# Kernel tuning notes

Hardware: AMD Instinct MI355X
Metric: run time of the kernel (lower is better)

The kernel has to match this reference:

```python
import jax, jax.numpy as jnp
import numpy as np
from jax import lax

# Quantization bit-widths per the module: QuantAct(16) on input,
# QuantConv2d(precision[0]=8), QuantAct(precision[0]+3=11) after relu1,
# QuantLinear(precision[1]=8).
INPUT_BIT = 16
CONV_W_BIT = 8
RELU_BIT = 11
DENSE_W_BIT = 8
EPS = 1e-8


def round_ste(x):
    # straight-through estimator rounding (HAWQ SymmetricQuantFunction)
    return x + lax.stop_gradient(jnp.round(x) - x)


def quant_act(x, bit):
    """Per-tensor symmetric dynamic activation quantization (HAWQ QuantAct).
    Returns fake-quantized x and its scaling factor."""
    n = 2 ** (bit - 1) - 1
    scale = lax.stop_gradient(jnp.maximum(jnp.max(jnp.abs(x)), EPS) / n)
    x_q = jnp.clip(round_ste(x / scale), -n, n) * scale
    return x_q, scale


def quant_weight(w, bit):
    """Per-output-channel symmetric weight quantization. w: [out, ...].
    Returns integer-valued weights and per-channel scale [out]."""
    n = 2 ** (bit - 1) - 1
    absmax = jnp.max(jnp.abs(w.reshape(w.shape[0], -1)), axis=1)
    sf = lax.stop_gradient(jnp.maximum(absmax, EPS) / n)
    bshape = (w.shape[0],) + (1,) * (w.ndim - 1)
    w_int = jnp.clip(round_ste(w / sf.reshape(bshape)), -n, n)
    return w_int, sf


def quant_conv2d(x, p_sf, w, b, bit, stride, pad):
    w_int, w_sf = quant_weight(w, bit)          # [O,I,kh,kw], [O]
    x_int = x / p_sf                            # integer-valued activations
    out_int = lax.conv_general_dilated(
        x_int, w_int, window_strides=(stride, stride),
        padding=((pad, pad), (pad, pad)),
        dimension_numbers=("NCHW", "OIHW", "NCHW"))
    bias_sf = p_sf * w_sf                       # [O]
    b_int = round_ste(b / bias_sf)
    out = (out_int + b_int[None, :, None, None]) * bias_sf[None, :, None, None]
    return out, w_sf


def quant_linear(x, p_sf, w, b, bit):
    w_int, w_sf = quant_weight(w, bit)          # [O,I], [O]
    x_int = x / p_sf
    bias_sf = p_sf * w_sf                       # [O]
    b_int = round_ste(b / bias_sf)
    out = (jnp.einsum("bi,oi->bo", x_int, w_int) + b_int[None, :]) * bias_sf[None, :]
    return out


def setup_inputs() -> dict:
    key = jax.random.key(0)
    k1, k2, k3, k4, k5 = jax.random.split(key, 5)
    B, Cin, H, W = 256, 3, 64, 64
    Cout, K = 64, 3
    Fin, Fout = Cout * 32 * 32, 256  # stride-2 conv -> 32x32 spatial
    x = jax.random.normal(k1, (B, Cin, H, W), dtype=jnp.float32)
    conv_w = jax.random.normal(k2, (Cout, Cin, K, K), dtype=jnp.float32) * 0.1
    conv_b = jax.random.normal(k3, (Cout,), dtype=jnp.float32) * 0.01
    dense_w = jax.random.normal(k4, (Fout, Fin), dtype=jnp.float32) * 0.02
    dense_b = jax.random.normal(k5, (Fout,), dtype=jnp.float32) * 0.01
    return {"x": x, "conv_w": conv_w, "conv_b": conv_b,
            "dense_w": dense_w, "dense_b": dense_b}


def reference(x, conv_w, conv_b, dense_w, dense_b):
    # x, p_sf = quant_input(x)
    xq, p_sf = quant_act(x, INPUT_BIT)
    # x, w_sf = conv(x, p_sf)
    h, w_sf = quant_conv2d(xq, p_sf, conv_w, conv_b, CONV_W_BIT, stride=2, pad=1)
    # relu1
    h = jax.nn.relu(h)
    # x, p_sf = quant_relu(x, p_sf, w_sf)  (requantize at relu_bit)
    h, p_sf = quant_act(h, RELU_BIT)
    # flatten
    h = h.reshape(h.shape[0], -1)
    # relu2(enc_dense(x, p_sf))
    out = jax.nn.relu(quant_linear(h, p_sf, dense_w, dense_b, DENSE_W_BIT))
    return out
```

## Files before the change

kernel.cpp:

```cpp
#include <hip/hip_runtime.h>
#include <hip/hip_fp16.h>
#include <cstdint>

#define B_   256
#define CIN  3
#define HW_  64
#define COUT 64
#define FIN  65536
#define FOUT 256

#define ACC_F    0
#define SC_F     65536
#define XPART_F  65552
#define WPART_F  66064
#define CSF_F    67088
#define CWINT_F  67152
#define H16_BYTE (512*1024)
#define WQ_BYTE  (H16_BYTE + 256ll*FIN*2)

typedef _Float16 half8  __attribute__((ext_vector_type(8)));
typedef _Float16 half4v __attribute__((ext_vector_type(4)));
typedef float    floatx4 __attribute__((ext_vector_type(4)));
typedef unsigned short u16;
typedef unsigned int uint_;

__device__ inline float blockMax(float v) {
    #pragma unroll
    for (int off = 32; off; off >>= 1) v = fmaxf(v, __shfl_down(v, off));
    __shared__ float sm[8];
    const int lane = threadIdx.x & 63, w = threadIdx.x >> 6;
    if (lane == 0) sm[w] = v;
    __syncthreads();
    float m = sm[0];
    const int nw = blockDim.x >> 6;
    for (int i = 1; i < nw; i++) m = fmaxf(m, sm[i]);
    return m;
}

__global__ __launch_bounds__(256) void k_stats(const float* __restrict__ x,
                                               const float* __restrict__ dw,
                                               const float* __restrict__ cw,
                                               float* __restrict__ ws) {
    const int b = blockIdx.x;
    const int t = threadIdx.x;
    if (b < 512) {
        const float4* x4 = (const float4*)x;
        float m = 0.f;
        for (int i = b * 256 + t; i < (B_ * CIN * HW_ * HW_) / 4; i += 512 * 256) {
            float4 v = x4[i];
            m = fmaxf(m, fmaxf(fmaxf(fabsf(v.x), fabsf(v.y)), fmaxf(fabsf(v.z), fabsf(v.w))));
        }
        float bm = blockMax(m);
        if (t == 0) ws[XPART_F + b] = bm;
    } else if (b < 1536) {
        const int b2 = b - 512;
        const int row = b2 >> 2, q = b2 & 3;
        const float4* r = (const float4*)(dw + (size_t)row * FIN) + q * 4096;
        float m = 0.f;
        for (int i = t; i < 4096; i += 256) {
            float4 v = r[i];
            m = fmaxf(m, fmaxf(fmaxf(fabsf(v.x), fabsf(v.y)), fmaxf(fabsf(v.z), fabsf(v.w))));
        }
        float bm = blockMax(m);
        if (t == 0) ws[WPART_F + b2] = bm;
    } else if (b == 1536) {
        if (t == 64) ((unsigned*)ws)[SC_F + 1] = 0u;
        if (t < 64) {
            const int o = t;
            float wv[27];
            float m = 0.f;
            #pragma unroll
            for (int i = 0; i < 27; i++) { wv[i] = cw[o * 27 + i]; m = fmaxf(m, fabsf(wv[i])); }
            const float sf = fmaxf(m, 1e-8f) / 127.0f;
            #pragma unroll
            for (int i = 0; i < 27; i++)
                ws[CWINT_F + o * 27 + i] = fminf(127.f, fmaxf(-127.f, rintf(wv[i] / sf)));
            ws[CSF_F + o] = sf;
        }
    } else {
        ws[ACC_F + (b - 1537) * 256 + t] = 0.f;
    }
}

__global__ __launch_bounds__(256) void k_conv(const float* __restrict__ x,
                                              const float* __restrict__ dw,
                                              const float* __restrict__ cb,
                                              const float* __restrict__ ws,
                                              u16* __restrict__ h16,
                                              signed char* __restrict__ wq,
                                              unsigned* __restrict__ maxh) {
    const int t = threadIdx.x;
    if (blockIdx.x >= 2048) {
        const int b2 = blockIdx.x - 2048;
        const int row = b2 >> 2, q = b2 & 3;
        const float* wp = ws + WPART_F + row * 4;
        const float am = fmaxf(fmaxf(wp[0], wp[1]), fmaxf(wp[2], wp[3]));
        const float inv = 127.0f / fmaxf(am, 1e-8f);
        const float4* r4 = (const float4*)(dw + (size_t)row * FIN) + q * 4096;
        uint_* wrow = (uint_*)(wq + (size_t)row * FIN) + q * 4096;
        for (int i = t; i < 4096; i += 256) {
            float4 v = r4[i];
            int q0 = (int)fminf(127.f, fmaxf(-127.f, rintf(v.x * inv)));
            int q1 = (int)fminf(127.f, fmaxf(-127.f, rintf(v.y * inv)));
            int q2 = (int)fminf(127.f, fmaxf(-127.f, rintf(v.z * inv)));
            int q3 = (int)fminf(127.f, fmaxf(-127.f, rintf(v.w * inv)));
            wrow[i] = (uint_)(q0 & 255) | ((uint_)(q1 & 255) << 8) |
                      ((uint_)(q2 & 255) << 16) | ((uint_)(q3 & 255) << 24);
        }
        return;
    }

    __shared__ float s_bsf[64], s_bint[64];
    __shared__ float xt[27 * 68];
    __shared__ float xp[256 * 28];

    float pm = fmaxf(ws[XPART_F + t], ws[XPART_F + 256 + t]);
    pm = blockMax(pm);
    const float p_sf = fmaxf(pm, 1e-8f) / 32767.0f;
    const float inv_p = 1.0f / p_sf;
    if (t < 64) {
        const float bsf = p_sf * ws[CSF_F + t];
        s_bsf[t]  = bsf;
        s_bint[t] = rintf(cb[t] / bsf);
    }

    const int b   = blockIdx.x >> 3;
    const int oyt = (blockIdx.x & 7) * 4;
    const float* xb = x + (size_t)b * (CIN * HW_ * HW_);

    for (int i = t; i < 432; i += 256) {
        const int lrow = i >> 4, c4 = i & 15;
        const int ci = lrow / 9, lr = lrow - ci * 9;
        const int iy = 2 * oyt - 1 + lr;
        float4 v = make_float4(0.f, 0.f, 0.f, 0.f);
        if ((unsigned)iy < 64u) v = *(const float4*)(xb + (ci * HW_ + iy) * HW_ + c4 * 4);
        float* d = &xt[lrow * 68 + 1 + c4 * 4];
        d[0] = fminf(32767.f, fmaxf(-32767.f, rintf(v.x * inv_p)));
        d[1] = fminf(32767.f, fmaxf(-32767.f, rintf(v.y * inv_p)));
        d[2] = fminf(32767.f, fmaxf(-32767.f, rintf(v.z * inv_p)));
        d[3] = fminf(32767.f, fmaxf(-32767.f, rintf(v.w * inv_p)));
    }
    if (t < 27) xt[t * 68] = 0.f;
    else if (t < 54) xt[(t - 27) * 68 + 65] = 0.f;
    __syncthreads();

    const int ox = t & 31;
    const int ch = __builtin_amdgcn_readfirstlane((t >> 6) & 1);
    const int dy = ((t >> 7) << 1) + ((t >> 5) & 1);
    const int oy = oyt + dy;

    float* myp = &xp[t * 28];
    #pragma unroll
    for (int ci = 0; ci < 3; ci++)
        #pragma unroll
        for (int ky = 0; ky < 3; ky++) {
            const float* rowp = &xt[(ci * 9 + 2 * dy + ky) * 68 + 2 * ox];
            #pragma unroll
            for (int kx = 0; kx < 3; kx++)
                myp[ci * 9 + ky * 3 + kx] = rowp[kx];
        }
    floatx4 xv0 = *(const floatx4*)(myp + 0);
    floatx4 xv1 = *(const floatx4*)(myp + 4);
    floatx4 xv2 = *(const floatx4*)(myp + 8);
    floatx4 xv3 = *(const floatx4*)(myp + 12);
    floatx4 xv4 = *(const floatx4*)(myp + 16);
    floatx4 xv5 = *(const floatx4*)(myp + 20);
    floatx4 xv6 = *(const floatx4*)(myp + 24);
    asm volatile("" : "+v"(xv0), "+v"(xv1), "+v"(xv2), "+v"(xv3),
                      "+v"(xv4), "+v"(xv5), "+v"(xv6));
    float xs[27];
    #pragma unroll
    for (int k = 0; k < 27; k++) {
        const int q = k >> 2, r = k & 3;
        xs[k] = (q == 0) ? xv0[r] : (q == 1) ? xv1[r] : (q == 2) ? xv2[r] :
                (q == 3) ? xv3[r] : (q == 4) ? xv4[r] : (q == 5) ? xv5[r] : xv6[r];
    }

    const float* wr = ws + CWINT_F + ch * (32 * 27);
    float mx = 0.f;
    u16* outp = h16 + (size_t)b * FIN + (size_t)ch * 32 * 1024 + oy * 32 + ox;

    float wbuf[27];
    #pragma unroll
    for (int k = 0; k < 27; k++) wbuf[k] = wr[k];
    #pragma unroll
    for (int c = 0; c < 32; c++) {
        float wcur[27];
        #pragma unroll
        for (int k = 0; k < 27; k++) wcur[k] = wbuf[k];
        if (c < 31) {
            const float* wn = wr + (c + 1) * 27;
            #pragma unroll
            for (int k = 0; k < 27; k++) wbuf[k] = wn[k];
        }
        float a = 0.f;
        #pragma unroll
        for (int k = 0; k < 27; k++) a = fmaf(xs[k], wcur[k], a);
        const int co = ch * 32 + c;
        float h = (a + s_bint[co]) * s_bsf[co];
        h = fmaxf(h, 0.f);
        mx = fmaxf(mx, h);
        outp[(size_t)c * 1024] = __half_as_ushort(__float2half(h));
    }
    float bm = blockMax(mx);
    if (t == 0) atomicMax(maxh, __float_as_uint(bm));
}

__device__ __forceinline__ half8 cvt_b8(uint_ lo, uint_ hi) {
    half8 h;
    h[0] = (_Float16)(float)(int)(signed char)(lo);
    h[1] = (_Float16)(float)(int)(signed char)(lo >> 8);
    h[2] = (_Float16)(float)(int)(signed char)(lo >> 16);
    h[3] = (_Float16)(float)(int)(signed char)(lo >> 24);
    h[4] = (_Float16)(float)(int)(signed char)(hi);
    h[5] = (_Float16)(float)(int)(signed char)(hi >> 8);
    h[6] = (_Float16)(float)(int)(signed char)(hi >> 16);
    h[7] = (_Float16)(float)(int)(signed char)(hi >> 24);
    return h;
}

__global__ __launch_bounds__(256) void k_gemm(const u16* __restrict__ h16,
                                              const signed char* __restrict__ wq,
                                              const float* __restrict__ ws,
                                              float* __restrict__ accb) {
    __shared__ __align__(16) _Float16 As[128][72];
    __shared__ __align__(16) _Float16 Bs[128][72];

    const int tid = threadIdx.x;
    const int tm  = (blockIdx.x >> 1) * 128;
    const int tn  = (blockIdx.x & 1) * 128;
    const int k0  = blockIdx.y * 1024;

    const float max_h  = __uint_as_float(((const unsigned*)ws)[SC_F + 1]);
    const float p2     = fmaxf(max_h, 1e-8f) / 1023.0f;
    const float inv_p2 = 1.0f / p2;

    floatx4 acc[4][4];
    const floatx4 zz = {0.f, 0.f, 0.f, 0.f};
    #pragma unroll
    for (int i = 0; i < 4; i++)
        #pragma unroll
        for (int j = 0; j < 4; j++) acc[i][j] = zz;

    const int wv = tid >> 6, lane = tid & 63;
    const int wm = (wv >> 1) * 64, wn = (wv & 1) * 64;
    const int lm = lane & 15, quad = lane >> 4;

    const int arow = tid >> 3, acol = tid & 7;
    const int brow = tid >> 1, bq   = (tid & 1) * 32;
    const u16* abase = h16 + (size_t)(tm + arow) * FIN + k0 + acol * 8;
    const signed char* bbase = wq + (size_t)(tn + brow) * FIN + k0 + bq;

#define LOADA(dst, kk) { _Pragma("unroll") \
    for (int r = 0; r < 4; r++) \
        dst[r] = *(const half8*)(abase + (size_t)r * 32 * FIN + (kk) * 64); }
#define LOADB(dst, kk) { const uint4* p_ = (const uint4*)(bbase + (kk) * 64); \
    dst[0] = p_[0]; dst[1] = p_[1]; }
#define STAGEA(src) { _Pragma("unroll") \
    for (int r = 0; r < 4; r++) { half8 qv; _Pragma("unroll") \
        for (int j = 0; j < 8; j++) { float f_ = (float)src[r][j]; \
            qv[j] = (_Float16)fminf(1023.f, rintf(f_ * inv_p2)); } \
        *(half8*)&As[arow + r * 32][acol * 8] = qv; } }
#define STAGEB(src) { _Pragma("unroll") \
    for (int u = 0; u < 2; u++) { uint4 wd_ = src[u]; \
        *(half8*)&Bs[brow][bq + u * 16 + 0] = cvt_b8(wd_.x, wd_.y); \
        *(half8*)&Bs[brow][bq + u * 16 + 8] = cvt_b8(wd_.z, wd_.w); } }
#define BARRIER() do { asm volatile("s_waitcnt lgkmcnt(0)" ::: "memory"); \
    __builtin_amdgcn_s_barrier(); } while (0)
#define MFMA_PHASE() { _Pragma("unroll") \
    for (int ks = 0; ks < 2; ks++) { half8 af[4], bf[4]; _Pragma("unroll") \
        for (int mi = 0; mi < 4; mi++) \
            af[mi] = *(const half8*)&As[wm + mi * 16 + lm][ks * 32 + quad * 8]; \
        _Pragma("unroll") \
        for (int ni = 0; ni < 4; ni++) \
            bf[ni] = *(const half8*)&Bs[wn + ni * 16 + lm][ks * 32 + quad * 8]; \
        _Pragma("unroll") \
        for (int mi = 0; mi < 4; mi++) _Pragma("unroll") \
            for (int ni = 0; ni < 4; ni++) \
                acc[mi][ni] = __builtin_amdgcn_mfma_f32_16x16x32_f16(af[mi], bf[ni], acc[mi][ni], 0, 0, 0); } }

    half8 a0[4], a1[4];
    uint4 b0[2], b1[2];

    LOADA(a0, 0); LOADB(b0, 0);
    LOADA(a1, 1); LOADB(b1, 1);

    for (int it = 0; it < 8; ++it) {
        STAGEA(a0); STAGEB(b0);
        if (it < 7) { LOADA(a0, 2 * it + 2); LOADB(b0, 2 * it + 2); }
        BARRIER();
        MFMA_PHASE();
        BARRIER();
        STAGEA(a1); STAGEB(b1);
        if (it < 7) { LOADA(a1, 2 * it + 3); LOADB(b1, 2 * it + 3); }
        BARRIER();
        MFMA_PHASE();
        BARRIER();
    }

    #pragma unroll
    for (int mi = 0; mi < 4; mi++)
        #pragma unroll
        for (int ni = 0; ni < 4; ni++)
            #pragma unroll
            for (int r = 0; r < 4; r++) {
                const int row = tm + wm + mi * 16 + quad * 4 + r;
                const int col = tn + wn + ni * 16 + lm;
                atomicAdd(accb + row * FOUT + col, acc[mi][ni][r]);
            }
#undef LOADA
#undef LOADB
#undef STAGEA
#undef STAGEB
#undef BARRIER
#undef MFMA_PHASE
}

__global__ void k_epi(const float* __restrict__ accb, const float* __restrict__ db,
                      const float* __restrict__ ws, float* __restrict__ out) {
    const int idx = blockIdx.x * 256 + threadIdx.x;
    const int n = idx & 255;
    const float max_h = __uint_as_float(((const unsigned*)ws)[SC_F + 1]);
    const float p2 = fmaxf(max_h, 1e-8f) / 1023.0f;
    const float* wp = ws + WPART_F + (size_t)n * 4;
    const float am = fmaxf(fmaxf(fmaxf(wp[0], wp[1]), fmaxf(wp[2], wp[3])), 1e-8f);
    const float wsf = am / 127.0f;
    const float bsf = p2 * wsf;
    const float bint = rintf(db[n] / bsf);
    out[idx] = fmaxf(0.f, (accb[idx] + bint) * bsf);
}

extern "C" void kernel_launch(void* const* d_in, const int* in_sizes, int n_in,
                              void* d_out, int out_size, void* d_ws, size_t ws_size,
                              hipStream_t stream) {
    (void)in_sizes; (void)n_in; (void)out_size; (void)ws_size;
    const float* x  = (const float*)d_in[0];
    const float* cw = (const float*)d_in[1];
    const float* cb = (const float*)d_in[2];
    const float* dw = (const float*)d_in[3];
    const float* db = (const float*)d_in[4];
    float* out = (float*)d_out;
    float* ws  = (float*)d_ws;
    u16* h16   = (u16*)((char*)d_ws + H16_BYTE);
    signed char* wq = (signed char*)d_ws + WQ_BYTE;
    float* accb = ws + ACC_F;
    unsigned* maxh = (unsigned*)ws + SC_F + 1;

    k_stats<<<1793, 256, 0, stream>>>(x, dw, cw, ws);
    k_conv<<<3072, 256, 0, stream>>>(x, dw, cb, ws, h16, wq, maxh);
    k_gemm<<<dim3(4, 64), 256, 0, stream>>>(h16, wq, ws, accb);
    k_epi<<<256, 256, 0, stream>>>(accb, db, ws, out);
}
```

Measured before the change: 191.0 us.

## Fuse epilogue into GEMM via last-block ticket and interleave conv/weight-quant blocks

```diff
diff --git a/kernel.cpp b/kernel.cpp
--- a/kernel.cpp
+++ b/kernel.cpp
@@ -65,6 +65,7 @@
         if (t == 0) ws[WPART_F + b2] = bm;
     } else if (b == 1536) {
         if (t == 64) ((unsigned*)ws)[SC_F + 1] = 0u;
+        if (t == 65) ((unsigned*)ws)[SC_F + 3] = 0u;
         if (t < 64) {
             const int o = t;
             float wv[27];
@@ -90,8 +91,9 @@
                                               signed char* __restrict__ wq,
                                               unsigned* __restrict__ maxh) {
     const int t = threadIdx.x;
-    if (blockIdx.x >= 2048) {
-        const int b2 = blockIdx.x - 2048;
+    const int bid = blockIdx.x;
+    if (bid % 3 == 2) {
+        const int b2 = bid / 3;
         const int row = b2 >> 2, q = b2 & 3;
         const float* wp = ws + WPART_F + row * 4;
         const float am = fmaxf(fmaxf(wp[0], wp[1]), fmaxf(wp[2], wp[3]));
@@ -109,6 +111,7 @@
         }
         return;
     }
+    const int cid = bid - bid / 3;
 
     __shared__ float s_bsf[64], s_bint[64];
     __shared__ float xt[27 * 68];
@@ -124,8 +127,8 @@
         s_bint[t] = rintf(cb[t] / bsf);
     }
 
-    const int b   = blockIdx.x >> 3;
-    const int oyt = (blockIdx.x & 7) * 4;
+    const int b   = cid >> 3;
+    const int oyt = (cid & 7) * 4;
     const float* xb = x + (size_t)b * (CIN * HW_ * HW_);
 
     for (int i = t; i < 432; i += 256) {
@@ -222,7 +225,10 @@
 __global__ __launch_bounds__(256) void k_gemm(const u16* __restrict__ h16,
                                               const signed char* __restrict__ wq,
                                               const float* __restrict__ ws,
-                                              float* __restrict__ accb) {
+                                              float* __restrict__ accb,
+                                              const float* __restrict__ db,
+                                              float* __restrict__ out,
+                                              unsigned* __restrict__ tick) {
     __shared__ __align__(16) _Float16 As[128][72];
     __shared__ __align__(16) _Float16 Bs[128][72];
 
@@ -314,20 +320,30 @@
 #undef STAGEB
 #undef BARRIER
 #undef MFMA_PHASE
-}
-
-__global__ void k_epi(const float* __restrict__ accb, const float* __restrict__ db,
-                      const float* __restrict__ ws, float* __restrict__ out) {
-    const int idx = blockIdx.x * 256 + threadIdx.x;
-    const int n = idx & 255;
-    const float max_h = __uint_as_float(((const unsigned*)ws)[SC_F + 1]);
-    const float p2 = fmaxf(max_h, 1e-8f) / 1023.0f;
-    const float* wp = ws + WPART_F + (size_t)n * 4;
-    const float am = fmaxf(fmaxf(fmaxf(wp[0], wp[1]), fmaxf(wp[2], wp[3])), 1e-8f);
-    const float wsf = am / 127.0f;
-    const float bsf = p2 * wsf;
-    const float bint = rintf(db[n] / bsf);
-    out[idx] = fmaxf(0.f, (accb[idx] + bint) * bsf);
+
+    __threadfence();
+    __shared__ unsigned s_tick;
+    if (tid == 0) s_tick = atomicAdd(tick, 1u);
+    __syncthreads();
+    if (s_tick != 255u) return;
+    __threadfence();
+    const float4* a4 = (const float4*)accb;
+    float4* o4 = (float4*)out;
+    for (int i = tid; i < (B_ * FOUT) / 4; i += 256) {
+        float4 v = a4[i];
+        float r[4] = {v.x, v.y, v.z, v.w};
+        float4 ov;
+        #pragma unroll
+        for (int j = 0; j < 4; j++) {
+            const int n = (i * 4 + j) & 255;
+            const float* wp = ws + WPART_F + n * 4;
+            const float am = fmaxf(fmaxf(fmaxf(wp[0], wp[1]), fmaxf(wp[2], wp[3])), 1e-8f);
+            const float bsf = p2 * (am / 127.0f);
+            const float bint = rintf(db[n] / bsf);
+            ((float*)&ov)[j] = fmaxf(0.f, (r[j] + bint) * bsf);
+        }
+        o4[i] = ov;
+    }
 }
 
 extern "C" void kernel_launch(void* const* d_in, const int* in_sizes, int n_in,
@@ -345,9 +361,9 @@
     signed char* wq = (signed char*)d_ws + WQ_BYTE;
     float* accb = ws + ACC_F;
     unsigned* maxh = (unsigned*)ws + SC_F + 1;
+    unsigned* tick = (unsigned*)ws + SC_F + 3;
 
     k_stats<<<1793, 256, 0, stream>>>(x, dw, cw, ws);
     k_conv<<<3072, 256, 0, stream>>>(x, dw, cb, ws, h16, wq, maxh);
-    k_gemm<<<dim3(4, 64), 256, 0, stream>>>(h16, wq, ws, accb);
-    k_epi<<<256, 256, 0, stream>>>(accb, db, ws, out);
-}
+    k_gemm<<<dim3(4, 64), 256, 0, stream>>>(h16, wq, ws, accb, db, out, tick);
+}
```

Measured after the change: 233.3 us. 22.2% more time.
